# Optimization experiments

Measured on AMD Instinct MI355X. Metric: run time of the kernel, lower is better.

Reference implementation:

```python
import jax, jax.numpy as jnp
import numpy as np

N, D, M, E, K = 16384, 512, 1024, 8, 2
LOSS_COEF = 0.01
EPS = 1e-10


def setup_inputs() -> dict:
    key = jax.random.key(0)
    ks = jax.random.split(key, 6)
    x = jax.random.normal(ks[0], (N, D), dtype=jnp.float32)
    # gate weight (torch init is zeros; use small random so routing is non-degenerate)
    w_gate = 0.02 * jax.random.normal(ks[1], (D, E), dtype=jnp.float32)
    # stacked expert FFN params: Linear(D->M), GELU, Linear(M->D)
    W1 = jax.random.normal(ks[2], (E, D, M), dtype=jnp.float32) / np.sqrt(D)
    b1 = jnp.zeros((E, M), dtype=jnp.float32)
    W2 = jax.random.normal(ks[3], (E, M, D), dtype=jnp.float32) / np.sqrt(M)
    b2 = jnp.zeros((E, D), dtype=jnp.float32)
    return {"x": x, "w_gate": w_gate, "W1": W1, "b1": b1, "W2": W2, "b2": b2}


def _cv_squared(v):
    # torch .var() is unbiased (ddof=1)
    v = v.astype(jnp.float32)
    return jnp.var(v, ddof=1) / (jnp.mean(v) ** 2 + EPS)


def reference(x, w_gate, W1, b1, W2, b2):
    n = x.shape[0]
    # --- noisy_top_k_gating (eval path: no noise) ---
    logits = x @ w_gate                                  # [N, E]
    top_logits, top_idx = jax.lax.top_k(logits, min(K + 1, E))
    topk_logits = top_logits[:, :K]                      # [N, K]
    topk_idx = top_idx[:, :K]                            # [N, K]
    topk_gates = jax.nn.softmax(topk_logits, axis=-1)    # [N, K]
    gates = jnp.zeros_like(logits).at[jnp.arange(n)[:, None], topk_idx].set(topk_gates)
    importance = gates.sum(axis=0)                       # [E]
    load = (gates > 0).sum(axis=0).astype(jnp.float32)   # [E]
    loss = LOSS_COEF * (_cv_squared(importance) + _cv_squared(load))
    # --- experts (dense equivalent of sparse dispatch/combine: gate==0 rows contribute 0) ---
    h = jnp.einsum('nd,edm->enm', x, W1) + b1[:, None, :]     # [E, N, M]
    h = jax.nn.gelu(h, approximate=False)
    out = jnp.einsum('enm,emd->end', h, W2) + b2[:, None, :]  # [E, N, D]
    y = jnp.einsum('ne,end->nd', gates, out)                  # [N, D]
    return (y, loss)
```

## Files before the change

### kernel.cpp

```cpp
#include <hip/hip_runtime.h>
#include <math.h>

#define NTOK 16384
#define DDIM 512
#define MDIM 1024
#define NEXP 8
#define LDSW 32
#define TMAX 264

typedef __attribute__((ext_vector_type(8))) short short8;
typedef __attribute__((ext_vector_type(4))) float floatx4;

__device__ inline unsigned short f2bf(float f){
  union { float f; unsigned int u; } v; v.f = f;
  unsigned int u = v.u;
  u += ((u >> 16) & 1u) + 0x7fffu;
  return (unsigned short)(u >> 16);
}

__device__ inline float bf2f(unsigned short s){
  union { unsigned int u; float f; } v;
  v.u = ((unsigned int)s) << 16;
  return v.f;
}

__device__ inline float gelu_fast(float x){
  float u = x * 0.70710678118654752f;
  float a = fabsf(u);
  float t = __builtin_amdgcn_rcpf(fmaf(0.3275911f, a, 1.0f));
  float p = fmaf(1.061405429f, t, -1.453152027f);
  p = fmaf(p, t, 1.421413741f);
  p = fmaf(p, t, -0.284496736f);
  p = fmaf(p, t, 0.254829592f);
  p = p * t;
  float e = __expf(-u * u);
  float erfa = fmaf(-p, e, 1.0f);
  float erfu = copysignf(erfa, u);
  return 0.5f * x * (1.0f + erfu);
}

__device__ __forceinline__ void gload16(const unsigned short* g, unsigned short* l){
  __builtin_amdgcn_global_load_lds(
      (const __attribute__((address_space(1))) void*)g,
      (__attribute__((address_space(3))) void*)l,
      16, 0, 0);
}


__global__ void init_small_kernel(int* counts, float* imp){
  int t = threadIdx.x;
  if (t < NEXP){ counts[t] = 0; imp[t] = 0.0f; }
}

__global__ void transpose_conv_kernel(const float* __restrict__ in,
                                      unsigned short* __restrict__ out,
                                      int R, int C){
  __shared__ float tile[32][33];
  int e  = blockIdx.z;
  int c0 = blockIdx.x << 5;
  int r0 = blockIdx.y << 5;
  const float* src = in + (size_t)e * R * C;
  unsigned short* dst = out + (size_t)e * R * C;
  int tc = threadIdx.x;
  int tr = threadIdx.y;
  #pragma unroll
  for (int i = 0; i < 32; i += 8)
    tile[tr + i][tc] = src[(size_t)(r0 + tr + i) * C + c0 + tc];
  __syncthreads();
  #pragma unroll
  for (int i = 0; i < 32; i += 8)
    dst[(size_t)(c0 + tr + i) * R + r0 + tc] = f2bf(tile[tc][tr + i]);
}


__global__ __launch_bounds__(256)
void gating_kernel(const float* __restrict__ x,
                   const float* __restrict__ wg,
                   unsigned short* __restrict__ xb,
                   int* __restrict__ tok_e, float* __restrict__ tok_g,
                   int* __restrict__ counts, float* __restrict__ imp){
  __shared__ int   lcnt[NEXP];
  __shared__ float limp[NEXP];
  int t = threadIdx.x;
  if (t < NEXP){ lcnt[t] = 0; limp[t] = 0.0f; }
  __syncthreads();

  int wave = t >> 6;
  int lane = t & 63;

  for (int it = 0; it < 4; it++){
    int n = blockIdx.x * 16 + it * 4 + wave;

    const float4* xp = (const float4*)(x + (size_t)n * DDIM + lane * 8);
    float4 a = xp[0], b = xp[1];
    float xv[8] = {a.x, a.y, a.z, a.w, b.x, b.y, b.z, b.w};

    short8 xo;
    #pragma unroll
    for (int j = 0; j < 8; j++) xo[j] = (short)f2bf(xv[j]);
    *(short8*)(xb + (size_t)n * DDIM + lane * 8) = xo;

    double acc[NEXP];
    #pragma unroll
    for (int e = 0; e < NEXP; e++) acc[e] = 0.0;
    #pragma unroll
    for (int j = 0; j < 8; j++){
      const float* wr = wg + (size_t)(lane * 8 + j) * NEXP;
      #pragma unroll
      for (int e = 0; e < NEXP; e++) acc[e] += (double)xv[j] * (double)wr[e];
    }
    #pragma unroll
    for (int off = 32; off >= 1; off >>= 1){
      #pragma unroll
      for (int e = 0; e < NEXP; e++) acc[e] += __shfl_xor(acc[e], off);
    }
    if (lane == 0){
      int i0 = -1, i1 = -1;
      double l0 = -1e300, l1 = -1e300;
      #pragma unroll
      for (int e = 0; e < NEXP; e++){
        double v = acc[e];
        if (v > l0){ l1 = l0; i1 = i0; l0 = v; i0 = e; }
        else if (v > l1){ l1 = v; i1 = e; }
      }
      float ex = expf((float)(l1 - l0));
      float g0 = 1.0f / (1.0f + ex);
      float g1 = ex / (1.0f + ex);
      tok_e[n * 2]     = i0; tok_e[n * 2 + 1] = i1;
      tok_g[n * 2]     = g0; tok_g[n * 2 + 1] = g1;
      atomicAdd(&lcnt[i0], 1); atomicAdd(&lcnt[i1], 1);
      atomicAdd(&limp[i0], g0); atomicAdd(&limp[i1], g1);
    }
  }
  __syncthreads();
  if (t < NEXP){
    atomicAdd(&counts[t], lcnt[t]);
    atomicAdd(&imp[t], limp[t]);
  }
}

__global__ void loss_scan_kernel(const int* __restrict__ counts,
                                 const float* __restrict__ imp,
                                 int* __restrict__ offsets, int* __restrict__ cursor,
                                 int* __restrict__ tile_pre,
                                 float* __restrict__ out_loss){
  int off = 0, tp = 0;
  double si = 0, si2 = 0, sl = 0, sl2 = 0;
  for (int e = 0; e < NEXP; e++){
    offsets[e] = off; cursor[e] = off;
    tile_pre[e] = tp;
    tp += (counts[e] + 127) >> 7;
    off += counts[e];
    double im = (double)imp[e];
    double ld = (double)counts[e];
    si += im; si2 += im * im;
    sl += ld; sl2 += ld * ld;
  }
  offsets[NEXP] = off;
  tile_pre[NEXP] = tp;
  double mi = si / 8.0, ml = sl / 8.0;
  double vi = (si2 - 8.0 * mi * mi) / 7.0;
  double vl = (sl2 - 8.0 * ml * ml) / 7.0;
  double loss = 0.01 * (vi / (mi * mi + 1e-10) + vl / (ml * ml + 1e-10));
  *out_loss = (float)loss;
}

__global__ __launch_bounds__(256)
void scatter_kernel(const int* __restrict__ tok_e,
                    int* __restrict__ cursor,
                    int* __restrict__ btok, int* __restrict__ slot_of){
  __shared__ int lcnt[NEXP];
  __shared__ int lbase[NEXP];
  int t = threadIdx.x;
  if (t < NEXP) lcnt[t] = 0;
  __syncthreads();

  int n = blockIdx.x * 256 + t;
  int e0 = tok_e[n * 2], e1 = tok_e[n * 2 + 1];
  int r0 = atomicAdd(&lcnt[e0], 1);
  int r1 = atomicAdd(&lcnt[e1], 1);
  __syncthreads();
  if (t < NEXP) lbase[t] = atomicAdd(&cursor[t], lcnt[t]);
  __syncthreads();
  int s0 = lbase[e0] + r0;
  int s1 = lbase[e1] + r1;
  btok[s0] = n;
  btok[s1] = n;
  slot_of[n * 2]     = s0;
  slot_of[n * 2 + 1] = s1;
}


__device__ __forceinline__ void stage_step(const unsigned short* aptr0, const unsigned short* aptr1,
                                           const unsigned short* bptr0, const unsigned short* bptr1,
                                           int k0, unsigned short* Ab, unsigned short* Bb, int wbase){
  gload16(aptr0 + k0, Ab + wbase);
  gload16(aptr1 + k0, Ab + 2048 + wbase);
  gload16(bptr0 + k0, Bb + wbase);
  gload16(bptr1 + k0, Bb + 2048 + wbase);
}

__device__ __forceinline__ void mfma_step(const unsigned short* A, const unsigned short* B,
                                          const int* aoff, const int* boff,
                                          floatx4 acc[4][4]){
  short8 af[4], bfrag[4];
  #pragma unroll
  for (int i = 0; i < 4; i++) af[i] = *(const short8*)(A + aoff[i]);
  #pragma unroll
  for (int j = 0; j < 4; j++) bfrag[j] = *(const short8*)(B + boff[j]);
  #pragma unroll
  for (int i = 0; i < 4; i++)
    #pragma unroll
    for (int j = 0; j < 4; j++)
      acc[i][j] = __builtin_amdgcn_mfma_f32_16x16x32_bf16(af[i], bfrag[j], acc[i][j], 0, 0, 0);
}

__global__ __launch_bounds__(256)
void gemm1_kernel(const unsigned short* __restrict__ xb,
                  const unsigned short* __restrict__ w1t,
                  const float* __restrict__ b1,
                  const int* __restrict__ offsets,
                  const int* __restrict__ tile_pre,
                  const int* __restrict__ btok,
                  unsigned short* __restrict__ H){
  int b = blockIdx.x;
  int L = (b & 7) * TMAX + (b >> 3);
  int ct = L & 7;
  int tt = L >> 3;
  if (tt >= tile_pre[NEXP]) return;
  int e = 0;
  while (tt >= tile_pre[e + 1]) e++;
  int rt = tt - tile_pre[e];
  int off = offsets[e];
  int cnt = offsets[e + 1] - off;
  int r0 = rt << 7;

  __shared__ unsigned short As[2][128 * LDSW];
  __shared__ unsigned short Bs[2][128 * LDSW];

  int t = threadIdx.x;
  int srow = t >> 2;
  int scol = (t & 3) << 3;
  int w = t >> 6;

  int ra0 = r0 + srow;        if (ra0 >= cnt) ra0 = cnt - 1;
  int ra1 = r0 + 64 + srow;   if (ra1 >= cnt) ra1 = cnt - 1;
  const unsigned short* aptr0 = xb + (size_t)btok[off + ra0] * DDIM + scol;
  const unsigned short* aptr1 = xb + (size_t)btok[off + ra1] * DDIM + scol;
  const unsigned short* bptr0 = w1t + ((size_t)e * MDIM + (ct << 7) + srow) * DDIM + scol;
  const unsigned short* bptr1 = bptr0 + (size_t)64 * DDIM;

  int wbase = w * 512;

  int lane = t & 63;
  int wr = (w >> 1) << 6;
  int wc = (w & 1) << 6;
  int lm = lane & 15;
  int lq = lane >> 4;

  int aoff[4], boff[4];
  #pragma unroll
  for (int i = 0; i < 4; i++){
    aoff[i] = (wr + i * 16 + lm) * LDSW + lq * 8;
    boff[i] = (wc + i * 16 + lm) * LDSW + lq * 8;
  }

  floatx4 acc[4][4] = {};

  stage_step(aptr0, aptr1, bptr0, bptr1, 0, As[0], Bs[0], wbase);
  __syncthreads();
  for (int k0 = 0; k0 < DDIM; k0 += 64){
    if (k0 + 32 < DDIM)
      stage_step(aptr0, aptr1, bptr0, bptr1, k0 + 32, As[1], Bs[1], wbase);
    mfma_step(As[0], Bs[0], aoff, boff, acc);
    __syncthreads();
    if (k0 + 64 < DDIM)
      stage_step(aptr0, aptr1, bptr0, bptr1, k0 + 64, As[0], Bs[0], wbase);
    mfma_step(As[1], Bs[1], aoff, boff, acc);
    __syncthreads();
  }

  const float* bias = b1 + e * MDIM + (ct << 7);
  #pragma unroll
  for (int i = 0; i < 4; i++){
    int rbase = wr + i * 16 + lq * 4;
    #pragma unroll
    for (int j = 0; j < 4; j++){
      int cc = wc + j * 16 + lm;
      float bv = bias[cc];
      #pragma unroll
      for (int r = 0; r < 4; r++){
        int row = r0 + rbase + r;
        if (row < cnt){
          float v = acc[i][j][r] + bv;
          H[(size_t)(off + row) * MDIM + (ct << 7) + cc] = f2bf(gelu_fast(v));
        }
      }
    }
  }
}

__global__ __launch_bounds__(256)
void gemm2_kernel(const unsigned short* __restrict__ H,
                  const unsigned short* __restrict__ w2t,
                  const float* __restrict__ b2,
                  const int* __restrict__ offsets,
                  const int* __restrict__ tile_pre,
                  unsigned short* __restrict__ O){
  int b = blockIdx.x;
  int L = (b & 7) * (TMAX / 2) + (b >> 3);
  int ct = L & 3;
  int tt = L >> 2;
  if (tt >= tile_pre[NEXP]) return;
  int e = 0;
  while (tt >= tile_pre[e + 1]) e++;
  int rt = tt - tile_pre[e];
  int off = offsets[e];
  int cnt = offsets[e + 1] - off;
  int r0 = rt << 7;

  __shared__ unsigned short As[2][128 * LDSW];
  __shared__ unsigned short Bs[2][128 * LDSW];

  int t = threadIdx.x;
  int srow = t >> 2;
  int scol = (t & 3) << 3;
  int w = t >> 6;

  int ra0 = r0 + srow;        if (ra0 >= cnt) ra0 = cnt - 1;
  int ra1 = r0 + 64 + srow;   if (ra1 >= cnt) ra1 = cnt - 1;
  const unsigned short* aptr0 = H + (size_t)(off + ra0) * MDIM + scol;
  const unsigned short* aptr1 = H + (size_t)(off + ra1) * MDIM + scol;
  const unsigned short* bptr0 = w2t + ((size_t)e * DDIM + (ct << 7) + srow) * MDIM + scol;
  const unsigned short* bptr1 = bptr0 + (size_t)64 * MDIM;

  int wbase = w * 512;

  int lane = t & 63;
  int wr = (w >> 1) << 6;
  int wc = (w & 1) << 6;
  int lm = lane & 15;
  int lq = lane >> 4;

  int aoff[4], boff[4];
  #pragma unroll
  for (int i = 0; i < 4; i++){
    aoff[i] = (wr + i * 16 + lm) * LDSW + lq * 8;
    boff[i] = (wc + i * 16 + lm) * LDSW + lq * 8;
  }

  floatx4 acc[4][4] = {};

  stage_step(aptr0, aptr1, bptr0, bptr1, 0, As[0], Bs[0], wbase);
  __syncthreads();
  for (int k0 = 0; k0 < MDIM; k0 += 64){
    if (k0 + 32 < MDIM)
      stage_step(aptr0, aptr1, bptr0, bptr1, k0 + 32, As[1], Bs[1], wbase);
    mfma_step(As[0], Bs[0], aoff, boff, acc);
    __syncthreads();
    if (k0 + 64 < MDIM)
      stage_step(aptr0, aptr1, bptr0, bptr1, k0 + 64, As[0], Bs[0], wbase);
    mfma_step(As[1], Bs[1], aoff, boff, acc);
    __syncthreads();
  }

  const float* bias = b2 + e * DDIM + (ct << 7);
  #pragma unroll
  for (int i = 0; i < 4; i++){
    int rbase = wr + i * 16 + lq * 4;
    #pragma unroll
    for (int j = 0; j < 4; j++){
      int cc = wc + j * 16 + lm;
      float bv = bias[cc];
      #pragma unroll
      for (int r = 0; r < 4; r++){
        int row = r0 + rbase + r;
        if (row < cnt)
          O[(size_t)(off + row) * DDIM + (ct << 7) + cc] = f2bf(acc[i][j][r] + bv);
      }
    }
  }
}


__global__ __launch_bounds__(256)
void combine_kernel(const unsigned short* __restrict__ O,
                    const float* __restrict__ tok_g,
                    const int* __restrict__ slot_of,
                    float* __restrict__ y){
  int wave = threadIdx.x >> 6;
  int lane = threadIdx.x & 63;
  int n = blockIdx.x * 4 + wave;
  int s0 = slot_of[n * 2], s1 = slot_of[n * 2 + 1];
  float g0 = tok_g[n * 2], g1 = tok_g[n * 2 + 1];
  short8 a = *(const short8*)(O + (size_t)s0 * DDIM + lane * 8);
  short8 b = *(const short8*)(O + (size_t)s1 * DDIM + lane * 8);
  float4 o0, o1;
  float* po0 = (float*)&o0;
  float* po1 = (float*)&o1;
  #pragma unroll
  for (int j = 0; j < 4; j++){
    po0[j] = g0 * bf2f((unsigned short)a[j]) + g1 * bf2f((unsigned short)b[j]);
    po1[j] = g0 * bf2f((unsigned short)a[j + 4]) + g1 * bf2f((unsigned short)b[j + 4]);
  }
  float4* yp = (float4*)(y + (size_t)n * DDIM + lane * 8);
  yp[0] = o0;
  yp[1] = o1;
}


extern "C" void kernel_launch(void* const* d_in, const int* in_sizes, int n_in,
                              void* d_out, int out_size, void* d_ws, size_t ws_size,
                              hipStream_t stream){
  const float* x  = (const float*)d_in[0];
  const float* wg = (const float*)d_in[1];
  const float* W1 = (const float*)d_in[2];
  const float* b1 = (const float*)d_in[3];
  const float* W2 = (const float*)d_in[4];
  const float* b2 = (const float*)d_in[5];
  float* y = (float*)d_out;

  char* ws = (char*)d_ws;
  size_t o = 0;
  auto alloc = [&](size_t bytes)->char*{
    char* p = ws + o;
    o += (bytes + 255) & ~(size_t)255;
    return p;
  };
  unsigned short* xb   = (unsigned short*)alloc((size_t)NTOK * DDIM * 2);
  unsigned short* w1t  = (unsigned short*)alloc((size_t)NEXP * MDIM * DDIM * 2);
  unsigned short* w2t  = (unsigned short*)alloc((size_t)NEXP * DDIM * MDIM * 2);
  unsigned short* H    = (unsigned short*)alloc((size_t)NTOK * 2 * MDIM * 2);
  unsigned short* O    = (unsigned short*)alloc((size_t)NTOK * 2 * DDIM * 2);
  int*   btok    = (int*)  alloc((size_t)NTOK * 2 * 4);
  int*   slot_of = (int*)  alloc((size_t)NTOK * 2 * 4);
  int*   tok_e   = (int*)  alloc((size_t)NTOK * 2 * 4);
  float* tok_g   = (float*)alloc((size_t)NTOK * 2 * 4);
  int*   counts  = (int*)  alloc(64);
  float* imp     = (float*)alloc(64);
  int*   offsets = (int*)  alloc(64);
  int*   cursor  = (int*)  alloc(64);
  int*   tile_pre= (int*)  alloc(64);

  hipLaunchKernelGGL(init_small_kernel, dim3(1), dim3(64), 0, stream, counts, imp);
  hipLaunchKernelGGL(transpose_conv_kernel, dim3(MDIM / 32, DDIM / 32, NEXP), dim3(32, 8), 0, stream,
                     W1, w1t, DDIM, MDIM);
  hipLaunchKernelGGL(transpose_conv_kernel, dim3(DDIM / 32, MDIM / 32, NEXP), dim3(32, 8), 0, stream,
                     W2, w2t, MDIM, DDIM);
  hipLaunchKernelGGL(gating_kernel, dim3(NTOK / 16), dim3(256), 0, stream,
                     x, wg, xb, tok_e, tok_g, counts, imp);
  hipLaunchKernelGGL(loss_scan_kernel, dim3(1), dim3(1), 0, stream,
                     counts, imp, offsets, cursor, tile_pre, y + (size_t)NTOK * DDIM);
  hipLaunchKernelGGL(scatter_kernel, dim3(NTOK / 256), dim3(256), 0, stream,
                     tok_e, cursor, btok, slot_of);
  hipLaunchKernelGGL(gemm1_kernel, dim3(TMAX * 8), dim3(256), 0, stream,
                     xb, w1t, b1, offsets, tile_pre, btok, H);
  hipLaunchKernelGGL(gemm2_kernel, dim3(TMAX * 4), dim3(256), 0, stream,
                     H, w2t, b2, offsets, tile_pre, O);
  hipLaunchKernelGGL(combine_kernel, dim3(NTOK / 4), dim3(256), 0, stream,
                     O, tok_g, slot_of, y);
}
```

Before: 295.6 us.

## Use single-buffered 64-wide K tiles with XOR-swizzled LDS and new block mapping

Both expert GEMM kernels switch from a double-buffered 32-wide K staging scheme to a single 128x64 LDS tile per operand. Loads go to an XOR-swizzled layout so the MFMA fragment reads avoid LDS bank conflicts. Block-to-tile mapping is also changed so that neighbouring blocks share column tiles in a different order, which may change L2 reuse. The cost is that global-load latency is no longer overlapped with compute, because there is no double buffering and each step waits at a sync before its MFMAs.

Measured after the change: 325.0 us. 9.9% more time.

```diff
diff --git a/kernel.cpp b/kernel.cpp
--- a/kernel.cpp
+++ b/kernel.cpp
@@ -5,7 +5,7 @@
 #define DDIM 512
 #define MDIM 1024
 #define NEXP 8
-#define LDSW 32
+#define BKW 64
 #define TMAX 264
 
 typedef __attribute__((ext_vector_type(8))) short short8;
@@ -191,30 +191,6 @@
 }
 
 
-__device__ __forceinline__ void stage_step(const unsigned short* aptr0, const unsigned short* aptr1,
-                                           const unsigned short* bptr0, const unsigned short* bptr1,
-                                           int k0, unsigned short* Ab, unsigned short* Bb, int wbase){
-  gload16(aptr0 + k0, Ab + wbase);
-  gload16(aptr1 + k0, Ab + 2048 + wbase);
-  gload16(bptr0 + k0, Bb + wbase);
-  gload16(bptr1 + k0, Bb + 2048 + wbase);
-}
-
-__device__ __forceinline__ void mfma_step(const unsigned short* A, const unsigned short* B,
-                                          const int* aoff, const int* boff,
-                                          floatx4 acc[4][4]){
-  short8 af[4], bfrag[4];
-  #pragma unroll
-  for (int i = 0; i < 4; i++) af[i] = *(const short8*)(A + aoff[i]);
-  #pragma unroll
-  for (int j = 0; j < 4; j++) bfrag[j] = *(const short8*)(B + boff[j]);
-  #pragma unroll
-  for (int i = 0; i < 4; i++)
-    #pragma unroll
-    for (int j = 0; j < 4; j++)
-      acc[i][j] = __builtin_amdgcn_mfma_f32_16x16x32_bf16(af[i], bfrag[j], acc[i][j], 0, 0, 0);
-}
-
 __global__ __launch_bounds__(256)
 void gemm1_kernel(const unsigned short* __restrict__ xb,
                   const unsigned short* __restrict__ w1t,
@@ -224,9 +200,10 @@
                   const int* __restrict__ btok,
                   unsigned short* __restrict__ H){
   int b = blockIdx.x;
-  int L = (b & 7) * TMAX + (b >> 3);
-  int ct = L & 7;
-  int tt = L >> 3;
+  int x = b & 7;
+  int u = b >> 3;
+  int ct = u & 7;
+  int tt = ((u >> 3) << 3) | x;
   if (tt >= tile_pre[NEXP]) return;
   int e = 0;
   while (tt >= tile_pre[e + 1]) e++;
@@ -235,48 +212,58 @@
   int cnt = offsets[e + 1] - off;
   int r0 = rt << 7;
 
-  __shared__ unsigned short As[2][128 * LDSW];
-  __shared__ unsigned short Bs[2][128 * LDSW];
+  __shared__ unsigned short As[128 * BKW];
+  __shared__ unsigned short Bs[128 * BKW];
 
   int t = threadIdx.x;
-  int srow = t >> 2;
-  int scol = (t & 3) << 3;
   int w = t >> 6;
-
-  int ra0 = r0 + srow;        if (ra0 >= cnt) ra0 = cnt - 1;
-  int ra1 = r0 + 64 + srow;   if (ra1 >= cnt) ra1 = cnt - 1;
-  const unsigned short* aptr0 = xb + (size_t)btok[off + ra0] * DDIM + scol;
-  const unsigned short* aptr1 = xb + (size_t)btok[off + ra1] * DDIM + scol;
-  const unsigned short* bptr0 = w1t + ((size_t)e * MDIM + (ct << 7) + srow) * DDIM + scol;
-  const unsigned short* bptr1 = bptr0 + (size_t)64 * DDIM;
-
-  int wbase = w * 512;
+  int rp = t >> 3;
+  int cs = (t & 7) ^ (rp & 7);
+
+  const unsigned short* apt[4];
+  const unsigned short* bpt[4];
+  #pragma unroll
+  for (int i = 0; i < 4; i++){
+    int ra = r0 + i * 32 + rp;  if (ra >= cnt) ra = cnt - 1;
+    apt[i] = xb + (size_t)btok[off + ra] * DDIM + cs * 8;
+    bpt[i] = w1t + ((size_t)e * MDIM + (ct << 7) + i * 32 + rp) * DDIM + cs * 8;
+  }
 
   int lane = t & 63;
   int wr = (w >> 1) << 6;
   int wc = (w & 1) << 6;
   int lm = lane & 15;
   int lq = lane >> 4;
+  int h  = lm & 7;
 
   int aoff[4], boff[4];
   #pragma unroll
   for (int i = 0; i < 4; i++){
-    aoff[i] = (wr + i * 16 + lm) * LDSW + lq * 8;
-    boff[i] = (wc + i * 16 + lm) * LDSW + lq * 8;
+    aoff[i] = (wr + i * 16 + lm) * BKW + ((lq ^ h) << 3);
+    boff[i] = (wc + i * 16 + lm) * BKW + ((lq ^ h) << 3);
   }
 
   floatx4 acc[4][4] = {};
-
-  stage_step(aptr0, aptr1, bptr0, bptr1, 0, As[0], Bs[0], wbase);
-  __syncthreads();
-  for (int k0 = 0; k0 < DDIM; k0 += 64){
-    if (k0 + 32 < DDIM)
-      stage_step(aptr0, aptr1, bptr0, bptr1, k0 + 32, As[1], Bs[1], wbase);
-    mfma_step(As[0], Bs[0], aoff, boff, acc);
+  for (int k0 = 0; k0 < DDIM; k0 += BKW){
+    #pragma unroll
+    for (int i = 0; i < 4; i++){
+      gload16(apt[i] + k0, As + i * 2048 + w * 512);
+      gload16(bpt[i] + k0, Bs + i * 2048 + w * 512);
+    }
     __syncthreads();
-    if (k0 + 64 < DDIM)
-      stage_step(aptr0, aptr1, bptr0, bptr1, k0 + 64, As[0], Bs[0], wbase);
-    mfma_step(As[1], Bs[1], aoff, boff, acc);
+    #pragma unroll
+    for (int kk = 0; kk < 2; kk++){
+      short8 af[4], bfr[4];
+      #pragma unroll
+      for (int i = 0; i < 4; i++) af[i]  = *(const short8*)(As + (aoff[i] ^ (kk << 5)));
+      #pragma unroll
+      for (int j = 0; j < 4; j++) bfr[j] = *(const short8*)(Bs + (boff[j] ^ (kk << 5)));
+      #pragma unroll
+      for (int i = 0; i < 4; i++)
+        #pragma unroll
+        for (int j = 0; j < 4; j++)
+          acc[i][j] = __builtin_amdgcn_mfma_f32_16x16x32_bf16(af[i], bfr[j], acc[i][j], 0, 0, 0);
+    }
     __syncthreads();
   }
 
@@ -308,9 +295,10 @@
                   const int* __restrict__ tile_pre,
                   unsigned short* __restrict__ O){
   int b = blockIdx.x;
-  int L = (b & 7) * (TMAX / 2) + (b >> 3);
-  int ct = L & 3;
-  int tt = L >> 2;
+  int x = b & 7;
+  int u = b >> 3;
+  int ct = u & 3;
+  int tt = ((u >> 2) << 3) | x;
   if (tt >= tile_pre[NEXP]) return;
   int e = 0;
   while (tt >= tile_pre[e + 1]) e++;
@@ -319,48 +307,58 @@
   int cnt = offsets[e + 1] - off;
   int r0 = rt << 7;
 
-  __shared__ unsigned short As[2][128 * LDSW];
-  __shared__ unsigned short Bs[2][128 * LDSW];
+  __shared__ unsigned short As[128 * BKW];
+  __shared__ unsigned short Bs[128 * BKW];
 
   int t = threadIdx.x;
-  int srow = t >> 2;
-  int scol = (t & 3) << 3;
   int w = t >> 6;
-
-  int ra0 = r0 + srow;        if (ra0 >= cnt) ra0 = cnt - 1;
-  int ra1 = r0 + 64 + srow;   if (ra1 >= cnt) ra1 = cnt - 1;
-  const unsigned short* aptr0 = H + (size_t)(off + ra0) * MDIM + scol;
-  const unsigned short* aptr1 = H + (size_t)(off + ra1) * MDIM + scol;
-  const unsigned short* bptr0 = w2t + ((size_t)e * DDIM + (ct << 7) + srow) * MDIM + scol;
-  const unsigned short* bptr1 = bptr0 + (size_t)64 * MDIM;
-
-  int wbase = w * 512;
+  int rp = t >> 3;
+  int cs = (t & 7) ^ (rp & 7);
+
+  const unsigned short* apt[4];
+  const unsigned short* bpt[4];
+  #pragma unroll
+  for (int i = 0; i < 4; i++){
+    int ra = r0 + i * 32 + rp;  if (ra >= cnt) ra = cnt - 1;
+    apt[i] = H + (size_t)(off + ra) * MDIM + cs * 8;
+    bpt[i] = w2t + ((size_t)e * DDIM + (ct << 7) + i * 32 + rp) * MDIM + cs * 8;
+  }
 
   int lane = t & 63;
   int wr = (w >> 1) << 6;
   int wc = (w & 1) << 6;
   int lm = lane & 15;
   int lq = lane >> 4;
+  int h  = lm & 7;
 
   int aoff[4], boff[4];
   #pragma unroll
   for (int i = 0; i < 4; i++){
-    aoff[i] = (wr + i * 16 + lm) * LDSW + lq * 8;
-    boff[i] = (wc + i * 16 + lm) * LDSW + lq * 8;
+    aoff[i] = (wr + i * 16 + lm) * BKW + ((lq ^ h) << 3);
+    boff[i] = (wc + i * 16 + lm) * BKW + ((lq ^ h) << 3);
   }
 
   floatx4 acc[4][4] = {};
-
-  stage_step(aptr0, aptr1, bptr0, bptr1, 0, As[0], Bs[0], wbase);
-  __syncthreads();
-  for (int k0 = 0; k0 < MDIM; k0 += 64){
-    if (k0 + 32 < MDIM)
-      stage_step(aptr0, aptr1, bptr0, bptr1, k0 + 32, As[1], Bs[1], wbase);
-    mfma_step(As[0], Bs[0], aoff, boff, acc);
+  for (int k0 = 0; k0 < MDIM; k0 += BKW){
+    #pragma unroll
+    for (int i = 0; i < 4; i++){
+      gload16(apt[i] + k0, As + i * 2048 + w * 512);
+      gload16(bpt[i] + k0, Bs + i * 2048 + w * 512);
+    }
     __syncthreads();
-    if (k0 + 64 < MDIM)
-      stage_step(aptr0, aptr1, bptr0, bptr1, k0 + 64, As[0], Bs[0], wbase);
-    mfma_step(As[1], Bs[1], aoff, boff, acc);
+    #pragma unroll
+    for (int kk = 0; kk < 2; kk++){
+      short8 af[4], bfr[4];
+      #pragma unroll
+      for (int i = 0; i < 4; i++) af[i]  = *(const short8*)(As + (aoff[i] ^ (kk << 5)));
+      #pragma unroll
+      for (int j = 0; j < 4; j++) bfr[j] = *(const short8*)(Bs + (boff[j] ^ (kk << 5)));
+      #pragma unroll
+      for (int i = 0; i < 4; i++)
+        #pragma unroll
+        for (int j = 0; j < 4; j++)
+          acc[i][j] = __builtin_amdgcn_mfma_f32_16x16x32_bf16(af[i], bfr[j], acc[i][j], 0, 0, 0);
+    }
     __syncthreads();
   }
 
```

## Swizzle LDS tiles in expert GEMMs and tighten double-buffer barriers

Applied to the files above, without the earlier changes.

Both expert GEMM kernels now XOR-swizzle the 8-element column groups used when global-to-LDS loads are staged, and apply the matching swizzle to the MFMA fragment reads, to cut LDS bank conflicts. The row-to-wave mapping of the loads changes to match. The main loop is rebuilt as a single-barrier ping-pong with an explicit vmcnt(0) wait and sched_barrier fences in place of __syncthreads. This puts correctness on the load and read swizzles matching and on the hand-placed waits covering the async LDS loads.

After: 303.1 us. 1.03x slower.

```diff
diff --git a/kernel.cpp b/kernel.cpp
--- a/kernel.cpp
+++ b/kernel.cpp
@@ -5,7 +5,7 @@
 #define DDIM 512
 #define MDIM 1024
 #define NEXP 8
-#define LDSW 32
+#define BKW 32
 #define TMAX 264
 
 typedef __attribute__((ext_vector_type(8))) short short8;
@@ -191,30 +191,6 @@
 }
 
 
-__device__ __forceinline__ void stage_step(const unsigned short* aptr0, const unsigned short* aptr1,
-                                           const unsigned short* bptr0, const unsigned short* bptr1,
-                                           int k0, unsigned short* Ab, unsigned short* Bb, int wbase){
-  gload16(aptr0 + k0, Ab + wbase);
-  gload16(aptr1 + k0, Ab + 2048 + wbase);
-  gload16(bptr0 + k0, Bb + wbase);
-  gload16(bptr1 + k0, Bb + 2048 + wbase);
-}
-
-__device__ __forceinline__ void mfma_step(const unsigned short* A, const unsigned short* B,
-                                          const int* aoff, const int* boff,
-                                          floatx4 acc[4][4]){
-  short8 af[4], bfrag[4];
-  #pragma unroll
-  for (int i = 0; i < 4; i++) af[i] = *(const short8*)(A + aoff[i]);
-  #pragma unroll
-  for (int j = 0; j < 4; j++) bfrag[j] = *(const short8*)(B + boff[j]);
-  #pragma unroll
-  for (int i = 0; i < 4; i++)
-    #pragma unroll
-    for (int j = 0; j < 4; j++)
-      acc[i][j] = __builtin_amdgcn_mfma_f32_16x16x32_bf16(af[i], bfrag[j], acc[i][j], 0, 0, 0);
-}
-
 __global__ __launch_bounds__(256)
 void gemm1_kernel(const unsigned short* __restrict__ xb,
                   const unsigned short* __restrict__ w1t,
@@ -235,50 +211,83 @@
   int cnt = offsets[e + 1] - off;
   int r0 = rt << 7;
 
-  __shared__ unsigned short As[2][128 * LDSW];
-  __shared__ unsigned short Bs[2][128 * LDSW];
+  __shared__ unsigned short As[2 * 128 * BKW];
+  __shared__ unsigned short Bs[2 * 128 * BKW];
 
   int t = threadIdx.x;
-  int srow = t >> 2;
-  int scol = (t & 3) << 3;
   int w = t >> 6;
-
-  int ra0 = r0 + srow;        if (ra0 >= cnt) ra0 = cnt - 1;
-  int ra1 = r0 + 64 + srow;   if (ra1 >= cnt) ra1 = cnt - 1;
-  const unsigned short* aptr0 = xb + (size_t)btok[off + ra0] * DDIM + scol;
-  const unsigned short* aptr1 = xb + (size_t)btok[off + ra1] * DDIM + scol;
-  const unsigned short* bptr0 = w1t + ((size_t)e * MDIM + (ct << 7) + srow) * DDIM + scol;
-  const unsigned short* bptr1 = bptr0 + (size_t)64 * DDIM;
-
-  int wbase = w * 512;
+  int l = t & 63;
+  int lrow = l >> 2;
+  int g = (l & 3) ^ ((l >> 3) & 3);
+
+  const unsigned short* apt0;
+  const unsigned short* apt1;
+  {
+    int ra0 = r0 + (0 * 4 + w) * 16 + lrow; if (ra0 >= cnt) ra0 = cnt - 1;
+    int ra1 = r0 + (1 * 4 + w) * 16 + lrow; if (ra1 >= cnt) ra1 = cnt - 1;
+    apt0 = xb + (size_t)btok[off + ra0] * DDIM + g * 8;
+    apt1 = xb + (size_t)btok[off + ra1] * DDIM + g * 8;
+  }
+  const unsigned short* bpt0 = w1t + ((size_t)e * MDIM + (ct << 7) + w * 16 + lrow) * DDIM + g * 8;
+  const unsigned short* bpt1 = bpt0 + (size_t)64 * DDIM;
 
   int lane = t & 63;
   int wr = (w >> 1) << 6;
   int wc = (w & 1) << 6;
   int lm = lane & 15;
   int lq = lane >> 4;
+  int swz = (lm >> 1) & 3;
 
   int aoff[4], boff[4];
   #pragma unroll
   for (int i = 0; i < 4; i++){
-    aoff[i] = (wr + i * 16 + lm) * LDSW + lq * 8;
-    boff[i] = (wc + i * 16 + lm) * LDSW + lq * 8;
+    aoff[i] = (wr + i * 16 + lm) * BKW + ((lq ^ swz) << 3);
+    boff[i] = (wc + i * 16 + lm) * BKW + ((lq ^ swz) << 3);
   }
 
   floatx4 acc[4][4] = {};
 
-  stage_step(aptr0, aptr1, bptr0, bptr1, 0, As[0], Bs[0], wbase);
-  __syncthreads();
-  for (int k0 = 0; k0 < DDIM; k0 += 64){
-    if (k0 + 32 < DDIM)
-      stage_step(aptr0, aptr1, bptr0, bptr1, k0 + 32, As[1], Bs[1], wbase);
-    mfma_step(As[0], Bs[0], aoff, boff, acc);
-    __syncthreads();
-    if (k0 + 64 < DDIM)
-      stage_step(aptr0, aptr1, bptr0, bptr1, k0 + 64, As[0], Bs[0], wbase);
-    mfma_step(As[1], Bs[1], aoff, boff, acc);
-    __syncthreads();
-  }
+  #define STAGE1(K0, CB) {                                   \
+    unsigned short* Ac = As + ((CB) << 12);                  \
+    unsigned short* Bc = Bs + ((CB) << 12);                  \
+    gload16(apt0 + (K0), Ac + w * 512);                      \
+    gload16(apt1 + (K0), Ac + 2048 + w * 512);               \
+    gload16(bpt0 + (K0), Bc + w * 512);                      \
+    gload16(bpt1 + (K0), Bc + 2048 + w * 512);               \
+  }
+  #define COMPUTE1(CB) {                                     \
+    const unsigned short* Ac = As + ((CB) << 12);            \
+    const unsigned short* Bc = Bs + ((CB) << 12);            \
+    short8 af[4], bfr[4];                                    \
+    _Pragma("unroll")                                        \
+    for (int i = 0; i < 4; i++) af[i]  = *(const short8*)(Ac + aoff[i]); \
+    _Pragma("unroll")                                        \
+    for (int j = 0; j < 4; j++) bfr[j] = *(const short8*)(Bc + boff[j]); \
+    _Pragma("unroll")                                        \
+    for (int i = 0; i < 4; i++)                              \
+      _Pragma("unroll")                                      \
+      for (int j = 0; j < 4; j++)                            \
+        acc[i][j] = __builtin_amdgcn_mfma_f32_16x16x32_bf16(af[i], bfr[j], acc[i][j], 0, 0, 0); \
+  }
+
+  int cur = 0;
+  STAGE1(0, 0);
+  asm volatile("s_waitcnt vmcnt(0)" ::: "memory");
+  __builtin_amdgcn_sched_barrier(0);
+  __builtin_amdgcn_s_barrier();
+  __builtin_amdgcn_sched_barrier(0);
+  for (int k = 1; k < DDIM / BKW; k++){
+    STAGE1(k * BKW, cur ^ 1);
+    COMPUTE1(cur);
+    asm volatile("s_waitcnt vmcnt(0)" ::: "memory");
+    __builtin_amdgcn_sched_barrier(0);
+    __builtin_amdgcn_s_barrier();
+    __builtin_amdgcn_sched_barrier(0);
+    cur ^= 1;
+  }
+  COMPUTE1(cur);
+  #undef STAGE1
+  #undef COMPUTE1
 
   const float* bias = b1 + e * MDIM + (ct << 7);
   #pragma unroll
@@ -319,50 +328,83 @@
   int cnt = offsets[e + 1] - off;
   int r0 = rt << 7;
 
-  __shared__ unsigned short As[2][128 * LDSW];
-  __shared__ unsigned short Bs[2][128 * LDSW];
+  __shared__ unsigned short As[2 * 128 * BKW];
+  __shared__ unsigned short Bs[2 * 128 * BKW];
 
   int t = threadIdx.x;
-  int srow = t >> 2;
-  int scol = (t & 3) << 3;
   int w = t >> 6;
-
-  int ra0 = r0 + srow;        if (ra0 >= cnt) ra0 = cnt - 1;
-  int ra1 = r0 + 64 + srow;   if (ra1 >= cnt) ra1 = cnt - 1;
-  const unsigned short* aptr0 = H + (size_t)(off + ra0) * MDIM + scol;
-  const unsigned short* aptr1 = H + (size_t)(off + ra1) * MDIM + scol;
-  const unsigned short* bptr0 = w2t + ((size_t)e * DDIM + (ct << 7) + srow) * MDIM + scol;
-  const unsigned short* bptr1 = bptr0 + (size_t)64 * MDIM;
-
-  int wbase = w * 512;
+  int l = t & 63;
+  int lrow = l >> 2;
+  int g = (l & 3) ^ ((l >> 3) & 3);
+
+  const unsigned short* apt0;
+  const unsigned short* apt1;
+  {
+    int ra0 = r0 + w * 16 + lrow;        if (ra0 >= cnt) ra0 = cnt - 1;
+    int ra1 = r0 + 64 + w * 16 + lrow;   if (ra1 >= cnt) ra1 = cnt - 1;
+    apt0 = H + (size_t)(off + ra0) * MDIM + g * 8;
+    apt1 = H + (size_t)(off + ra1) * MDIM + g * 8;
+  }
+  const unsigned short* bpt0 = w2t + ((size_t)e * DDIM + (ct << 7) + w * 16 + lrow) * MDIM + g * 8;
+  const unsigned short* bpt1 = bpt0 + (size_t)64 * MDIM;
 
   int lane = t & 63;
   int wr = (w >> 1) << 6;
   int wc = (w & 1) << 6;
   int lm = lane & 15;
   int lq = lane >> 4;
+  int swz = (lm >> 1) & 3;
 
   int aoff[4], boff[4];
   #pragma unroll
   for (int i = 0; i < 4; i++){
-    aoff[i] = (wr + i * 16 + lm) * LDSW + lq * 8;
-    boff[i] = (wc + i * 16 + lm) * LDSW + lq * 8;
+    aoff[i] = (wr + i * 16 + lm) * BKW + ((lq ^ swz) << 3);
+    boff[i] = (wc + i * 16 + lm) * BKW + ((lq ^ swz) << 3);
   }
 
   floatx4 acc[4][4] = {};
 
-  stage_step(aptr0, aptr1, bptr0, bptr1, 0, As[0], Bs[0], wbase);
-  __syncthreads();
-  for (int k0 = 0; k0 < MDIM; k0 += 64){
-    if (k0 + 32 < MDIM)
-      stage_step(aptr0, aptr1, bptr0, bptr1, k0 + 32, As[1], Bs[1], wbase);
-    mfma_step(As[0], Bs[0], aoff, boff, acc);
-    __syncthreads();
-    if (k0 + 64 < MDIM)
-      stage_step(aptr0, aptr1, bptr0, bptr1, k0 + 64, As[0], Bs[0], wbase);
-    mfma_step(As[1], Bs[1], aoff, boff, acc);
-    __syncthreads();
-  }
+  #define STAGE2(K0, CB) {                                   \
+    unsigned short* Ac = As + ((CB) << 12);                  \
+    unsigned short* Bc = Bs + ((CB) << 12);                  \
+    gload16(apt0 + (K0), Ac + w * 512);                      \
+    gload16(apt1 + (K0), Ac + 2048 + w * 512);               \
+    gload16(bpt0 + (K0), Bc + w * 512);                      \
+    gload16(bpt1 + (K0), Bc + 2048 + w * 512);               \
+  }
+  #define COMPUTE2(CB) {                                     \
+    const unsigned short* Ac = As + ((CB) << 12);            \
+    const unsigned short* Bc = Bs + ((CB) << 12);            \
+    short8 af[4], bfr[4];                                    \
+    _Pragma("unroll")                                        \
+    for (int i = 0; i < 4; i++) af[i]  = *(const short8*)(Ac + aoff[i]); \
+    _Pragma("unroll")                                        \
+    for (int j = 0; j < 4; j++) bfr[j] = *(const short8*)(Bc + boff[j]); \
+    _Pragma("unroll")                                        \
+    for (int i = 0; i < 4; i++)                              \
+      _Pragma("unroll")                                      \
+      for (int j = 0; j < 4; j++)                            \
+        acc[i][j] = __builtin_amdgcn_mfma_f32_16x16x32_bf16(af[i], bfr[j], acc[i][j], 0, 0, 0); \
+  }
+
+  int cur = 0;
+  STAGE2(0, 0);
+  asm volatile("s_waitcnt vmcnt(0)" ::: "memory");
+  __builtin_amdgcn_sched_barrier(0);
+  __builtin_amdgcn_s_barrier();
+  __builtin_amdgcn_sched_barrier(0);
+  for (int k = 1; k < MDIM / BKW; k++){
+    STAGE2(k * BKW, cur ^ 1);
+    COMPUTE2(cur);
+    asm volatile("s_waitcnt vmcnt(0)" ::: "memory");
+    __builtin_amdgcn_sched_barrier(0);
+    __builtin_amdgcn_s_barrier();
+    __builtin_amdgcn_sched_barrier(0);
+    cur ^= 1;
+  }
+  COMPUTE2(cur);
+  #undef STAGE2
+  #undef COMPUTE2
 
   const float* bias = b2 + e * DDIM + (ct << 7);
   #pragma unroll
```
